# Performance work log

Measured on AMD Instinct MI355X. Metric: run time of the kernel, lower is better.

## Reference

```python
import jax, jax.numpy as jnp
import numpy as np
import math

B, I, O, SEG = 128, 2048, 2048, 10

def setup_inputs() -> dict:
    key = jax.random.key(0)
    k1, k2, k3, k4 = jax.random.split(key, 4)
    scale = 1.0 / math.sqrt(I)
    return {
        "x": jax.random.normal(k1, (B, I), dtype=jnp.float32),
        "context": jax.random.normal(k2, (O,), dtype=jnp.float32),
        "prev_activation": jax.random.normal(k3, (B, O), dtype=jnp.float32),
        "weight": jax.random.normal(k4, (O, I), dtype=jnp.float32) * scale,
        "bias": jnp.zeros((O,), dtype=jnp.float32),
        "astrocyte_activation": jnp.ones((O,), dtype=jnp.float32),
        "dendrite_segments": jax.random.normal(jax.random.fold_in(key, 7), (O, I, SEG), dtype=jnp.float32) * scale,
    }

def reference(x, context, prev_activation, weight, bias, astrocyte_activation, dendrite_segments):
    # Astrocyte gating of the linear weight: sigmoid(astro * context) -> [o]
    astro_mod = jax.nn.sigmoid(astrocyte_activation * context)
    # Dendritic branch: relu(einsum('bi,oij->boj')) summed over segments -> [b, o]
    dendritic_out = jnp.maximum(jnp.einsum('bi,oij->boj', x, dendrite_segments), 0.0).sum(axis=2)
    # Gated linear: F.linear(x, weight * astro_mod[:, None], bias) -> [b, o]
    out = x @ (weight * astro_mod[:, None]).T + bias
    # Note: torch's STDP/Hebbian weight mutations (synaptic_tag, protein_synthesis,
    # homeostatic scaling) occur AFTER 'out' is computed and do not affect the
    # returned tensor; they are pure parameter side effects, so omitted here.
    return out + dendritic_out
```

## Files before the change

kernel.cpp:

```cpp
#include <hip/hip_runtime.h>
#include <hip/hip_bf16.h>

#define B_ 128
#define I_ 2048
#define O_ 2048
#define SEG 10
#define BK 32
#define KSLICE 1024
#define NST (KSLICE / BK)
#define XTILE 8192
#define DCH 1280
#define DLS 1408

typedef __attribute__((ext_vector_type(8))) short bf16x8;
typedef __attribute__((ext_vector_type(4))) float f32x4;

static __device__ __forceinline__ unsigned short f2bf(float f) {
    unsigned u = __float_as_uint(f);
    u += 0x7FFFu + ((u >> 16) & 1u);
    return (unsigned short)(u >> 16);
}

#define GLDS16(SRC, DST) \
    __builtin_amdgcn_global_load_lds( \
        (const __attribute__((address_space(1))) unsigned*)(SRC), \
        (__attribute__((address_space(3))) unsigned*)(DST), 16, 0, 0)
#define GLDS4(SRC, DST) \
    __builtin_amdgcn_global_load_lds( \
        (const __attribute__((address_space(1))) unsigned*)(SRC), \
        (__attribute__((address_space(3))) unsigned*)(DST), 4, 0, 0)

__global__ void xconv(const float* __restrict__ x, char* __restrict__ xb) {
    int idx = blockIdx.x * 256 + threadIdx.x;
    int row = idx >> 8;
    int c   = idx & 255;
    int k0  = c * 8;
    int tt  = k0 >> 5;
    int kl  = k0 & 31;

    const float* xp = x + (size_t)row * I_ + k0;
    float4 a = *reinterpret_cast<const float4*>(xp);
    float4 b = *reinterpret_cast<const float4*>(xp + 4);

    bf16x8 h;
    h[0] = (short)f2bf(a.x); h[1] = (short)f2bf(a.y);
    h[2] = (short)f2bf(a.z); h[3] = (short)f2bf(a.w);
    h[4] = (short)f2bf(b.x); h[5] = (short)f2bf(b.y);
    h[6] = (short)f2bf(b.z); h[7] = (short)f2bf(b.w);

    int sw = ((row >> 1) & 3) << 4;
    size_t off = (size_t)tt * XTILE + row * 64 + ((kl * 2) ^ sw);
    *reinterpret_cast<bf16x8*>(xb + off) = h;
}

__global__ __launch_bounds__(256, 2) void neuro_fused(
    const char*  __restrict__ xb,
    const float* __restrict__ ctx,
    const float* __restrict__ w,
    const float* __restrict__ bias,
    const float* __restrict__ astro,
    const float* __restrict__ D,
    float* __restrict__ out)
{
    __shared__ __align__(16) char xs[2][2][XTILE];
    __shared__ __align__(16) char dls[4][2][2][DLS];

    const int tid  = threadIdx.x;
    const int wave = tid >> 6;
    const int lane = tid & 63;
    const int p    = wave >> 1;
    const int s    = wave & 1;
    const int o0   = blockIdx.x * 4 + p * 2;
    const int col  = lane & 15;
    const int g    = lane >> 4;

    f32x4 acc[2][8];
#pragma unroll
    for (int oo = 0; oo < 2; ++oo)
#pragma unroll
        for (int m = 0; m < 8; ++m) acc[oo][m] = (f32x4){0.f, 0.f, 0.f, 0.f};

    const int   fbase = (col < 10) ? col * 4 : DCH;
    const int   fstr  = (col < 10) ? 40 : 4;
    const float dmask = (col <= 10) ? 1.0f : 0.0f;
    const int   sw    = ((col >> 1) & 3) << 4;

    auto stage_x = [&](int t, int buf) {
        const char* src = xb + (size_t)(s * NST + t) * XTILE + p * 4096 + lane * 16;
        char* dst = &xs[s][buf][p * 4096];
#pragma unroll
        for (int c = 0; c < 4; ++c)
            GLDS16(src + c * 1024, dst + c * 1024);
    };

    auto stage_d = [&](int t, int buf) {
        const size_t krow = (size_t)(s * KSLICE + t * BK);
#pragma unroll
        for (int oo = 0; oo < 2; ++oo) {
            const char* srcD = (const char*)D + ((size_t)(o0 + oo) * (I_ * SEG) + krow * SEG) * 4;
            char* dst = &dls[wave][buf][oo][0];
            GLDS16(srcD + lane * 16, dst);
            GLDS4(srcD + 1024 + lane * 4, dst + 1024);
            const char* srcW = (const char*)w + ((size_t)(o0 + oo) * I_ + krow) * 4;
            if (lane < 32) GLDS4(srcW + lane * 4, dst + DCH);
        }
    };

    auto compute = [&](int buf) {
        const char* xbase = &xs[s][buf][0];
        bf16x8 af[8];
#pragma unroll
        for (int m = 0; m < 8; ++m)
            af[m] = *reinterpret_cast<const bf16x8*>(
                xbase + (m * 16 + col) * 64 + ((16 * g) ^ sw));
#pragma unroll
        for (int oo = 0; oo < 2; ++oo) {
            const char* fp = &dls[wave][buf][oo][0] + fbase + (8 * g) * fstr;
            bf16x8 bfrag;
#pragma unroll
            for (int e = 0; e < 8; ++e) {
                float v = *reinterpret_cast<const float*>(fp + e * fstr);
                bfrag[e] = (short)f2bf(v * dmask);
            }
#pragma unroll
            for (int m = 0; m < 8; ++m)
                acc[oo][m] = __builtin_amdgcn_mfma_f32_16x16x32_bf16(af[m], bfrag, acc[oo][m], 0, 0, 0);
        }
    };

    stage_x(0, 0);
    stage_d(0, 0);
    __syncthreads();

#pragma unroll 1
    for (int t = 0; t < NST; t += 2) {
        stage_x(t + 1, 1);
        stage_d(t + 1, 1);
        compute(0);
        __syncthreads();

        if (t + 2 < NST) {
            stage_x(t + 2, 0);
            stage_d(t + 2, 0);
        }
        compute(1);
        __syncthreads();
    }

    float* cs = reinterpret_cast<float*>(&xs[0][0][0]);
    if (s == 1) {
#pragma unroll
        for (int oo = 0; oo < 2; ++oo)
#pragma unroll
            for (int m = 0; m < 8; ++m)
                *reinterpret_cast<f32x4*>(cs + p * 4096 + (oo * 8 + m) * 256 + lane * 4) = acc[oo][m];
    }
    __syncthreads();
    if (s == 0) {
#pragma unroll
        for (int oo = 0; oo < 2; ++oo) {
            float am = astro[o0 + oo] * ctx[o0 + oo];
            am = 1.0f / (1.0f + __expf(-am));
            const float bo = bias[o0 + oo];
#pragma unroll
            for (int m = 0; m < 8; ++m) {
                f32x4 other = *reinterpret_cast<const f32x4*>(cs + p * 4096 + (oo * 8 + m) * 256 + lane * 4);
#pragma unroll
                for (int r = 0; r < 4; ++r) {
                    float v = acc[oo][m][r] + other[r];
                    float dend = (col < 10) ? fmaxf(v, 0.0f) : 0.0f;
#pragma unroll
                    for (int sh = 1; sh < 16; sh <<= 1)
                        dend += __shfl_xor(dend, sh, 64);
                    float lin = __shfl(v, (lane & 48) | 10, 64);
                    if (col == 0) {
                        int b = m * 16 + g * 4 + r;
                        out[(size_t)b * O_ + (o0 + oo)] = dend + am * lin + bo;
                    }
                }
            }
        }
    }
}

extern "C" void kernel_launch(void* const* d_in, const int* in_sizes, int n_in,
                              void* d_out, int out_size, void* d_ws, size_t ws_size,
                              hipStream_t stream) {
    const float* x     = (const float*)d_in[0];
    const float* ctx   = (const float*)d_in[1];
    const float* w     = (const float*)d_in[3];
    const float* bias  = (const float*)d_in[4];
    const float* astro = (const float*)d_in[5];
    const float* D     = (const float*)d_in[6];
    float* out = (float*)d_out;
    char* xb = (char*)d_ws;

    xconv<<<dim3(128), dim3(256), 0, stream>>>(x, xb);
    neuro_fused<<<dim3(512), dim3(256), 0, stream>>>(xb, ctx, w, bias, astro, D, out);
}
```

Baseline: 54.72 us.

## Keep two stages of async loads in flight using explicit vmcnt waits

The main loop now prefetches two K-stages ahead. It waits with s_waitcnt vmcnt(10), which covers exactly the older stage's ten global-to-LDS loads, and uses raw s_barrier with sched barriers. Before, __syncthreads drained every outstanding load each step. The aim is to keep more of the memory-bound dendrite-segment stream in flight and hide latency behind MFMA work. The sigmoid gate and bias loads are also hoisted to the kernel start. Correctness depends on the hand-counted vmcnt matching the compiler's emitted load count, including the lane-conditional weight load.

```diff
diff --git a/kernel.cpp b/kernel.cpp
--- a/kernel.cpp
+++ b/kernel.cpp
@@ -29,6 +29,11 @@
     __builtin_amdgcn_global_load_lds( \
         (const __attribute__((address_space(1))) unsigned*)(SRC), \
         (__attribute__((address_space(3))) unsigned*)(DST), 4, 0, 0)
+
+#define WAITVM(N) asm volatile("s_waitcnt vmcnt(" #N ")" ::: "memory")
+#define BARRIER() do { __builtin_amdgcn_sched_barrier(0); \
+                       __builtin_amdgcn_s_barrier(); \
+                       __builtin_amdgcn_sched_barrier(0); } while (0)
 
 __global__ void xconv(const float* __restrict__ x, char* __restrict__ xb) {
     int idx = blockIdx.x * 256 + threadIdx.x;
@@ -80,6 +85,13 @@
 #pragma unroll
         for (int m = 0; m < 8; ++m) acc[oo][m] = (f32x4){0.f, 0.f, 0.f, 0.f};
 
+    float am0 = astro[o0] * ctx[o0];
+    float am1 = astro[o0 + 1] * ctx[o0 + 1];
+    am0 = 1.0f / (1.0f + __expf(-am0));
+    am1 = 1.0f / (1.0f + __expf(-am1));
+    const float bo0 = bias[o0];
+    const float bo1 = bias[o0 + 1];
+
     const int   fbase = (col < 10) ? col * 4 : DCH;
     const int   fstr  = (col < 10) ? 40 : 4;
     const float dmask = (col <= 10) ? 1.0f : 0.0f;
@@ -128,25 +140,31 @@
         }
     };
 
-    stage_x(0, 0);
-    stage_d(0, 0);
+    stage_x(0, 0); stage_d(0, 0);
+    stage_x(1, 1); stage_d(1, 1);
+
+#pragma unroll 1
+    for (int t = 0; t < NST - 2; t += 2) {
+        WAITVM(10);
+        BARRIER();
+        compute(0);
+        BARRIER();
+        stage_x(t + 2, 0); stage_d(t + 2, 0);
+
+        WAITVM(10);
+        BARRIER();
+        compute(1);
+        BARRIER();
+        stage_x(t + 3, 1); stage_d(t + 3, 1);
+    }
+    WAITVM(10);
+    BARRIER();
+    compute(0);
+    WAITVM(0);
+    BARRIER();
+    compute(1);
+
     __syncthreads();
-
-#pragma unroll 1
-    for (int t = 0; t < NST; t += 2) {
-        stage_x(t + 1, 1);
-        stage_d(t + 1, 1);
-        compute(0);
-        __syncthreads();
-
-        if (t + 2 < NST) {
-            stage_x(t + 2, 0);
-            stage_d(t + 2, 0);
-        }
-        compute(1);
-        __syncthreads();
-    }
-
     float* cs = reinterpret_cast<float*>(&xs[0][0][0]);
     if (s == 1) {
 #pragma unroll
@@ -159,9 +177,8 @@
     if (s == 0) {
 #pragma unroll
         for (int oo = 0; oo < 2; ++oo) {
-            float am = astro[o0 + oo] * ctx[o0 + oo];
-            am = 1.0f / (1.0f + __expf(-am));
-            const float bo = bias[o0 + oo];
+            const float am = oo ? am1 : am0;
+            const float bo = oo ? bo1 : bo0;
 #pragma unroll
             for (int m = 0; m < 8; ++m) {
                 f32x4 other = *reinterpret_cast<const f32x4*>(cs + p * 4096 + (oo * 8 + m) * 256 + lane * 4);
```

After: 54.73 us. Within noise of the previous version (+0.0%).

## Halve outputs per block, deepen D-staging ring, use explicit vmcnt pipelining

Applied to the files above, without the earlier changes.

Each wave pair now handles one output neuron instead of two, and the grid doubles to 1024 blocks. Occupancy is raised to 3 blocks per CU. The per-wave dendrite/weight staging becomes a 3-slot ring, and the double-step loop is replaced by a single-step loop. That loop uses explicit s_waitcnt vmcnt and scheduling barriers, so one stage's global-to-LDS loads stay in flight while the current tile is computed. The aim is better latency hiding on this bandwidth-bound kernel, at the cost of reloading x tiles for twice as many blocks and relying on hand-counted vmcnt values.

```diff
diff --git a/kernel.cpp b/kernel.cpp
--- a/kernel.cpp
+++ b/kernel.cpp
@@ -10,7 +10,7 @@
 #define NST (KSLICE / BK)
 #define XTILE 8192
 #define DCH 1280
-#define DLS 1408
+#define DLS 1536
 
 typedef __attribute__((ext_vector_type(8))) short bf16x8;
 typedef __attribute__((ext_vector_type(4))) float f32x4;
@@ -29,6 +29,11 @@
     __builtin_amdgcn_global_load_lds( \
         (const __attribute__((address_space(1))) unsigned*)(SRC), \
         (__attribute__((address_space(3))) unsigned*)(DST), 4, 0, 0)
+
+#define WAITVM(N) asm volatile("s_waitcnt vmcnt(" #N ")" ::: "memory")
+#define BARRIER() do { __builtin_amdgcn_sched_barrier(0); \
+                       __builtin_amdgcn_s_barrier(); \
+                       __builtin_amdgcn_sched_barrier(0); } while (0)
 
 __global__ void xconv(const float* __restrict__ x, char* __restrict__ xb) {
     int idx = blockIdx.x * 256 + threadIdx.x;
@@ -53,7 +58,7 @@
     *reinterpret_cast<bf16x8*>(xb + off) = h;
 }
 
-__global__ __launch_bounds__(256, 2) void neuro_fused(
+__global__ __launch_bounds__(256, 3) void neuro_fused(
     const char*  __restrict__ xb,
     const float* __restrict__ ctx,
     const float* __restrict__ w,
@@ -63,27 +68,28 @@
     float* __restrict__ out)
 {
     __shared__ __align__(16) char xs[2][2][XTILE];
-    __shared__ __align__(16) char dls[4][2][2][DLS];
+    __shared__ __align__(16) char dls[4][3][DLS];
 
     const int tid  = threadIdx.x;
     const int wave = tid >> 6;
     const int lane = tid & 63;
     const int p    = wave >> 1;
     const int s    = wave & 1;
-    const int o0   = blockIdx.x * 4 + p * 2;
+    const int o    = blockIdx.x * 2 + p;
     const int col  = lane & 15;
     const int g    = lane >> 4;
 
-    f32x4 acc[2][8];
+    f32x4 acc[8];
 #pragma unroll
-    for (int oo = 0; oo < 2; ++oo)
-#pragma unroll
-        for (int m = 0; m < 8; ++m) acc[oo][m] = (f32x4){0.f, 0.f, 0.f, 0.f};
+    for (int m = 0; m < 8; ++m) acc[m] = (f32x4){0.f, 0.f, 0.f, 0.f};
 
-    const int   fbase = (col < 10) ? col * 4 : DCH;
-    const int   fstr  = (col < 10) ? 40 : 4;
-    const float dmask = (col <= 10) ? 1.0f : 0.0f;
-    const int   sw    = ((col >> 1) & 3) << 4;
+    float am = astro[o] * ctx[o];
+    am = 1.0f / (1.0f + __expf(-am));
+    const float bo = bias[o];
+
+    const int fbase = (col < 10) ? col * 4 : DCH;
+    const int fstr  = (col < 10) ? 40 : 4;
+    const int sw    = ((col >> 1) & 3) << 4;
 
     auto stage_x = [&](int t, int buf) {
         const char* src = xb + (size_t)(s * NST + t) * XTILE + p * 4096 + lane * 16;
@@ -93,90 +99,77 @@
             GLDS16(src + c * 1024, dst + c * 1024);
     };
 
-    auto stage_d = [&](int t, int buf) {
+    auto stage_d = [&](int t, int slot) {
         const size_t krow = (size_t)(s * KSLICE + t * BK);
-#pragma unroll
-        for (int oo = 0; oo < 2; ++oo) {
-            const char* srcD = (const char*)D + ((size_t)(o0 + oo) * (I_ * SEG) + krow * SEG) * 4;
-            char* dst = &dls[wave][buf][oo][0];
-            GLDS16(srcD + lane * 16, dst);
-            GLDS4(srcD + 1024 + lane * 4, dst + 1024);
-            const char* srcW = (const char*)w + ((size_t)(o0 + oo) * I_ + krow) * 4;
-            if (lane < 32) GLDS4(srcW + lane * 4, dst + DCH);
-        }
+        const char* srcD = (const char*)D + ((size_t)o * (I_ * SEG) + krow * SEG) * 4;
+        char* dst = &dls[wave][slot][0];
+        GLDS16(srcD + lane * 16, dst);
+        GLDS4(srcD + 1024 + lane * 4, dst + 1024);
+        const char* srcW = (const char*)w + ((size_t)o * I_ + krow) * 4;
+        if (lane < 32) GLDS4(srcW + lane * 4, dst + DCH);
     };
 
-    auto compute = [&](int buf) {
-        const char* xbase = &xs[s][buf][0];
+    auto compute = [&](int bufx, int slot) {
+        const char* xbase = &xs[s][bufx][0];
+        const char* dbase = &dls[wave][slot][0];
         bf16x8 af[8];
 #pragma unroll
         for (int m = 0; m < 8; ++m)
             af[m] = *reinterpret_cast<const bf16x8*>(
                 xbase + (m * 16 + col) * 64 + ((16 * g) ^ sw));
+        const char* fp = dbase + fbase + (8 * g) * fstr;
+        bf16x8 bfrag;
 #pragma unroll
-        for (int oo = 0; oo < 2; ++oo) {
-            const char* fp = &dls[wave][buf][oo][0] + fbase + (8 * g) * fstr;
-            bf16x8 bfrag;
+        for (int e = 0; e < 8; ++e) {
+            float v = *reinterpret_cast<const float*>(fp + e * fstr);
+            __hip_bfloat16 h = __float2bfloat16(v);
+            bfrag[e] = *reinterpret_cast<short*>(&h);
+        }
 #pragma unroll
-            for (int e = 0; e < 8; ++e) {
-                float v = *reinterpret_cast<const float*>(fp + e * fstr);
-                bfrag[e] = (short)f2bf(v * dmask);
-            }
-#pragma unroll
-            for (int m = 0; m < 8; ++m)
-                acc[oo][m] = __builtin_amdgcn_mfma_f32_16x16x32_bf16(af[m], bfrag, acc[oo][m], 0, 0, 0);
-        }
+        for (int m = 0; m < 8; ++m)
+            acc[m] = __builtin_amdgcn_mfma_f32_16x16x32_bf16(af[m], bfrag, acc[m], 0, 0, 0);
     };
 
-    stage_x(0, 0);
-    stage_d(0, 0);
-    __syncthreads();
+    stage_x(0, 0); stage_d(0, 0);
+    stage_x(1, 1); stage_d(1, 1);
 
+    int cslot = 0;
 #pragma unroll 1
-    for (int t = 0; t < NST; t += 2) {
-        stage_x(t + 1, 1);
-        stage_d(t + 1, 1);
-        compute(0);
-        __syncthreads();
-
+    for (int t = 0; t < NST; ++t) {
+        if (t < NST - 1) { WAITVM(7); } else { WAITVM(0); }
+        BARRIER();
+        compute(t & 1, cslot);
+        BARRIER();
         if (t + 2 < NST) {
-            stage_x(t + 2, 0);
-            stage_d(t + 2, 0);
+            stage_x(t + 2, t & 1);
+            stage_d(t + 2, cslot == 0 ? 2 : cslot - 1);
         }
-        compute(1);
-        __syncthreads();
+        cslot = (cslot == 2) ? 0 : cslot + 1;
     }
 
+    __syncthreads();
     float* cs = reinterpret_cast<float*>(&xs[0][0][0]);
     if (s == 1) {
 #pragma unroll
-        for (int oo = 0; oo < 2; ++oo)
-#pragma unroll
-            for (int m = 0; m < 8; ++m)
-                *reinterpret_cast<f32x4*>(cs + p * 4096 + (oo * 8 + m) * 256 + lane * 4) = acc[oo][m];
+        for (int m = 0; m < 8; ++m)
+            *reinterpret_cast<f32x4*>(cs + p * 2048 + m * 256 + lane * 4) = acc[m];
     }
     __syncthreads();
     if (s == 0) {
 #pragma unroll
-        for (int oo = 0; oo < 2; ++oo) {
-            float am = astro[o0 + oo] * ctx[o0 + oo];
-            am = 1.0f / (1.0f + __expf(-am));
-            const float bo = bias[o0 + oo];
+        for (int m = 0; m < 8; ++m) {
+            f32x4 other = *reinterpret_cast<const f32x4*>(cs + p * 2048 + m * 256 + lane * 4);
 #pragma unroll
-            for (int m = 0; m < 8; ++m) {
-                f32x4 other = *reinterpret_cast<const f32x4*>(cs + p * 4096 + (oo * 8 + m) * 256 + lane * 4);
+            for (int r = 0; r < 4; ++r) {
+                float v = acc[m][r] + other[r];
+                float dend = (col < 10) ? fmaxf(v, 0.0f) : 0.0f;
 #pragma unroll
-                for (int r = 0; r < 4; ++r) {
-                    float v = acc[oo][m][r] + other[r];
-                    float dend = (col < 10) ? fmaxf(v, 0.0f) : 0.0f;
-#pragma unroll
-                    for (int sh = 1; sh < 16; sh <<= 1)
-                        dend += __shfl_xor(dend, sh, 64);
-                    float lin = __shfl(v, (lane & 48) | 10, 64);
-                    if (col == 0) {
-                        int b = m * 16 + g * 4 + r;
-                        out[(size_t)b * O_ + (o0 + oo)] = dend + am * lin + bo;
-                    }
+                for (int sh = 1; sh < 16; sh <<= 1)
+                    dend += __shfl_xor(dend, sh, 64);
+                float lin = __shfl(v, (lane & 48) | 10, 64);
+                if (col == 0) {
+                    int b = m * 16 + g * 4 + r;
+                    out[(size_t)b * O_ + o] = dend + am * lin + bo;
                 }
             }
         }
@@ -196,5 +189,5 @@
     char* xb = (char*)d_ws;
 
     xconv<<<dim3(128), dim3(256), 0, stream>>>(x, xb);
-    neuro_fused<<<dim3(512), dim3(256), 0, stream>>>(xb, ctx, w, bias, astro, D, out);
+    neuro_fused<<<dim3(1024), dim3(256), 0, stream>>>(xb, ctx, w, bias, astro, D, out);
 }
```

Measured after the change: 70.00 us. +27.9%, slower.

## Warp-specialize producer/consumer waves with a four-stage LDS pipeline and no K split

Applied to the files above, without the earlier changes.

Splits each block into two producer waves that issue global-to-LDS loads and two consumer waves that run the MFMA compute. Loads run three stages ahead through a four-deep ring buffer, paced by explicit vmcnt waits and raw barriers. Each consumer now covers the full K range for two outputs, which removes the split-K LDS reduction, and the sigmoid and bias are computed up front. The bf16 conversion switches to packed pair conversion and the column mask is dropped. In exchange, only half the waves issue MFMAs, so each consumer runs twice as many iterations, and the hand-tuned waitcnt pacing is fragile.

```diff
diff --git a/kernel.cpp b/kernel.cpp
--- a/kernel.cpp
+++ b/kernel.cpp
@@ -6,8 +6,7 @@
 #define O_ 2048
 #define SEG 10
 #define BK 32
-#define KSLICE 1024
-#define NST (KSLICE / BK)
+#define NST (I_ / BK)
 #define XTILE 8192
 #define DCH 1280
 #define DLS 1408
@@ -19,6 +18,11 @@
     unsigned u = __float_as_uint(f);
     u += 0x7FFFu + ((u >> 16) & 1u);
     return (unsigned short)(u >> 16);
+}
+
+static __device__ __forceinline__ unsigned cvt2(float lo, float hi) {
+    __hip_bfloat162 h = __float22bfloat162_rn(make_float2(lo, hi));
+    return *reinterpret_cast<unsigned*>(&h);
 }
 
 #define GLDS16(SRC, DST) \
@@ -29,6 +33,11 @@
     __builtin_amdgcn_global_load_lds( \
         (const __attribute__((address_space(1))) unsigned*)(SRC), \
         (__attribute__((address_space(3))) unsigned*)(DST), 4, 0, 0)
+
+#define WAITVM(N) asm volatile("s_waitcnt vmcnt(" #N ")" ::: "memory")
+#define BARRIER() do { __builtin_amdgcn_sched_barrier(0); \
+                       __builtin_amdgcn_s_barrier(); \
+                       __builtin_amdgcn_sched_barrier(0); } while (0)
 
 __global__ void xconv(const float* __restrict__ x, char* __restrict__ xb) {
     int idx = blockIdx.x * 256 + threadIdx.x;
@@ -62,52 +71,63 @@
     const float* __restrict__ D,
     float* __restrict__ out)
 {
-    __shared__ __align__(16) char xs[2][2][XTILE];
-    __shared__ __align__(16) char dls[4][2][2][DLS];
+    __shared__ __align__(16) char xs[4][XTILE];
+    __shared__ __align__(16) char dls[4][4][DLS];
 
     const int tid  = threadIdx.x;
-    const int wave = tid >> 6;
+    const int wv   = tid >> 6;
     const int lane = tid & 63;
-    const int p    = wave >> 1;
-    const int s    = wave & 1;
-    const int o0   = blockIdx.x * 4 + p * 2;
+    const bool isP = (wv < 2);
+    const int o0   = blockIdx.x * 4;
     const int col  = lane & 15;
     const int g    = lane >> 4;
 
-    f32x4 acc[2][8];
-#pragma unroll
-    for (int oo = 0; oo < 2; ++oo)
-#pragma unroll
-        for (int m = 0; m < 8; ++m) acc[oo][m] = (f32x4){0.f, 0.f, 0.f, 0.f};
-
-    const int   fbase = (col < 10) ? col * 4 : DCH;
-    const int   fstr  = (col < 10) ? 40 : 4;
-    const float dmask = (col <= 10) ? 1.0f : 0.0f;
-    const int   sw    = ((col >> 1) & 3) << 4;
-
-    auto stage_x = [&](int t, int buf) {
-        const char* src = xb + (size_t)(s * NST + t) * XTILE + p * 4096 + lane * 16;
-        char* dst = &xs[s][buf][p * 4096];
+    const int p = wv;
+    auto stage_x = [&](int t) {
+        const char* src = xb + (size_t)t * XTILE + p * 4096 + lane * 16;
+        char* dst = &xs[t & 3][p * 4096];
 #pragma unroll
         for (int c = 0; c < 4; ++c)
             GLDS16(src + c * 1024, dst + c * 1024);
     };
-
-    auto stage_d = [&](int t, int buf) {
-        const size_t krow = (size_t)(s * KSLICE + t * BK);
-#pragma unroll
-        for (int oo = 0; oo < 2; ++oo) {
-            const char* srcD = (const char*)D + ((size_t)(o0 + oo) * (I_ * SEG) + krow * SEG) * 4;
-            char* dst = &dls[wave][buf][oo][0];
+    auto stage_d = [&](int t) {
+#pragma unroll
+        for (int q = 0; q < 2; ++q) {
+            const int ol = 2 * p + q;
+            const char* srcD = (const char*)D + (size_t)(o0 + ol) * (I_ * SEG * 4)
+                             + (size_t)t * DCH;
+            char* dst = &dls[ol][t & 3][0];
             GLDS16(srcD + lane * 16, dst);
             GLDS4(srcD + 1024 + lane * 4, dst + 1024);
-            const char* srcW = (const char*)w + ((size_t)(o0 + oo) * I_ + krow) * 4;
+            const char* srcW = (const char*)w + (size_t)(o0 + ol) * (I_ * 4) + t * (BK * 4);
             if (lane < 32) GLDS4(srcW + lane * 4, dst + DCH);
         }
     };
 
-    auto compute = [&](int buf) {
-        const char* xbase = &xs[s][buf][0];
+    const int c_ = wv - 2;
+    f32x4 acc[2][8];
+#pragma unroll
+    for (int oo = 0; oo < 2; ++oo)
+#pragma unroll
+        for (int m = 0; m < 8; ++m) acc[oo][m] = (f32x4){0.f, 0.f, 0.f, 0.f};
+
+    float am[2], bo[2];
+    if (!isP) {
+#pragma unroll
+        for (int oo = 0; oo < 2; ++oo) {
+            const int o = o0 + 2 * c_ + oo;
+            float a = astro[o] * ctx[o];
+            am[oo] = 1.0f / (1.0f + __expf(-a));
+            bo[oo] = bias[o];
+        }
+    }
+
+    const int fbase = (col < 10) ? col * 4 : DCH;
+    const int fstr  = (col < 10) ? 40 : 4;
+    const int sw    = ((col >> 1) & 3) << 4;
+
+    auto compute = [&](int u) {
+        const char* xbase = &xs[u & 3][0];
         bf16x8 af[8];
 #pragma unroll
         for (int m = 0; m < 8; ++m)
@@ -115,59 +135,50 @@
                 xbase + (m * 16 + col) * 64 + ((16 * g) ^ sw));
 #pragma unroll
         for (int oo = 0; oo < 2; ++oo) {
-            const char* fp = &dls[wave][buf][oo][0] + fbase + (8 * g) * fstr;
-            bf16x8 bfrag;
-#pragma unroll
-            for (int e = 0; e < 8; ++e) {
-                float v = *reinterpret_cast<const float*>(fp + e * fstr);
-                bfrag[e] = (short)f2bf(v * dmask);
-            }
+            const char* fp = &dls[2 * c_ + oo][u & 3][0] + fbase + (8 * g) * fstr;
+            float bv[8];
+#pragma unroll
+            for (int e = 0; e < 8; ++e)
+                bv[e] = *reinterpret_cast<const float*>(fp + e * fstr);
+            union { bf16x8 v; unsigned uu[4]; } bf;
+#pragma unroll
+            for (int e2 = 0; e2 < 4; ++e2)
+                bf.uu[e2] = cvt2(bv[2 * e2], bv[2 * e2 + 1]);
 #pragma unroll
             for (int m = 0; m < 8; ++m)
-                acc[oo][m] = __builtin_amdgcn_mfma_f32_16x16x32_bf16(af[m], bfrag, acc[oo][m], 0, 0, 0);
+                acc[oo][m] = __builtin_amdgcn_mfma_f32_16x16x32_bf16(af[m], bf.v, acc[oo][m], 0, 0, 0);
         }
     };
 
-    stage_x(0, 0);
-    stage_d(0, 0);
-    __syncthreads();
+    if (isP) {
+        stage_x(0); stage_d(0);
+        stage_x(1); stage_d(1);
+        stage_x(2); stage_d(2);
+        WAITVM(20);
+    }
 
 #pragma unroll 1
-    for (int t = 0; t < NST; t += 2) {
-        stage_x(t + 1, 1);
-        stage_d(t + 1, 1);
-        compute(0);
-        __syncthreads();
-
-        if (t + 2 < NST) {
-            stage_x(t + 2, 0);
-            stage_d(t + 2, 0);
-        }
-        compute(1);
-        __syncthreads();
-    }
-
-    float* cs = reinterpret_cast<float*>(&xs[0][0][0]);
-    if (s == 1) {
-#pragma unroll
-        for (int oo = 0; oo < 2; ++oo)
-#pragma unroll
-            for (int m = 0; m < 8; ++m)
-                *reinterpret_cast<f32x4*>(cs + p * 4096 + (oo * 8 + m) * 256 + lane * 4) = acc[oo][m];
-    }
-    __syncthreads();
-    if (s == 0) {
+    for (int u = 0; u < NST; ++u) {
+        BARRIER();
+        if (isP) {
+            if (u + 3 < NST) { stage_x(u + 3); stage_d(u + 3); }
+            if (u <= NST - 4)      { WAITVM(20); }
+            else if (u == NST - 3) { WAITVM(10); }
+            else                   { WAITVM(0);  }
+        } else {
+            compute(u);
+        }
+    }
+
+    if (!isP) {
 #pragma unroll
         for (int oo = 0; oo < 2; ++oo) {
-            float am = astro[o0 + oo] * ctx[o0 + oo];
-            am = 1.0f / (1.0f + __expf(-am));
-            const float bo = bias[o0 + oo];
+            const int o = o0 + 2 * c_ + oo;
 #pragma unroll
             for (int m = 0; m < 8; ++m) {
-                f32x4 other = *reinterpret_cast<const f32x4*>(cs + p * 4096 + (oo * 8 + m) * 256 + lane * 4);
 #pragma unroll
                 for (int r = 0; r < 4; ++r) {
-                    float v = acc[oo][m][r] + other[r];
+                    float v = acc[oo][m][r];
                     float dend = (col < 10) ? fmaxf(v, 0.0f) : 0.0f;
 #pragma unroll
                     for (int sh = 1; sh < 16; sh <<= 1)
@@ -175,7 +186,7 @@
                     float lin = __shfl(v, (lane & 48) | 10, 64);
                     if (col == 0) {
                         int b = m * 16 + g * 4 + r;
-                        out[(size_t)b * O_ + (o0 + oo)] = dend + am * lin + bo;
+                        out[(size_t)b * O_ + o] = dend + am[oo] * lin + bo[oo];
                     }
                 }
             }
```

Measured after the change: 48.94 us (median of 2 runs). 10.6% less time.
